# Optimization experiments

Hardware: AMD Instinct MI355X
Metric: run time of the kernel (lower is better)

## Reference

```python
import jax, jax.numpy as jnp
import numpy as np
import math

B, SES, SEQ, H, K = 16, 16, 64, 512, 32
L = SES * SEQ


def setup_inputs() -> dict:
    key = jax.random.key(0)
    ks = jax.random.split(key, 16)
    s = 1.0 / math.sqrt(H)
    return {
        "user_emb": jax.random.normal(ks[0], (B, H), jnp.float32),
        "item_emb": jax.random.normal(ks[1], (B, SES, SEQ, H), jnp.float32),
        "mask": jnp.zeros((B, L, K), jnp.float32),
        "index": jax.random.randint(ks[2], (L, K), 0, L, jnp.int64),
        "Wq": jax.random.normal(ks[3], (H, H), jnp.float32) * s,
        "bq": jnp.zeros((H,), jnp.float32),
        "Wk": jax.random.normal(ks[4], (H, H), jnp.float32) * s,
        "bk": jnp.zeros((H,), jnp.float32),
        "Wv": jax.random.normal(ks[5], (H, H), jnp.float32) * s,
        "bv": jnp.zeros((H,), jnp.float32),
        "Wd": jax.random.normal(ks[6], (H, H), jnp.float32) * s,
        "bd": jnp.zeros((H,), jnp.float32),
        "ln_g": jnp.ones((H,), jnp.float32),
        "ln_b": jnp.zeros((H,), jnp.float32),
    }


def reference(user_emb, item_emb, mask, index, Wq, bq, Wk, bk, Wv, bv, Wd, bd, ln_g, ln_b):
    b, ses, seq, h = item_emb.shape
    l = ses * seq
    item_flat = item_emb.reshape(b, l, h)
    q = user_emb @ Wq.T + bq                       # [B, H]
    k = item_flat @ Wk.T + bk                      # [B, L, H]
    v = item_flat @ Wv.T + bv                      # [B, L, H]
    # scalar query against all L keys, scaled by sqrt(hidden_size)
    scores = jnp.einsum("bh,blh->bl", q, k) / math.sqrt(h)
    scores = scores[:, index] + mask               # gather -> [B, L, K]
    w = jax.nn.softmax(scores, axis=-1)            # [B, L, K]
    vg = v[:, index, :]                            # gather -> [B, L, K, H]
    attn_out = jnp.einsum("blk,blkh->blh", w, vg)  # [B, L, H]
    dense = attn_out @ Wd.T + bd
    x = dense + item_flat                          # residual (dropout = identity, eval)
    mu = jnp.mean(x, axis=-1, keepdims=True)
    var = jnp.var(x, axis=-1, keepdims=True)
    y = (x - mu) / jnp.sqrt(var + 1e-12) * ln_g + ln_b
    return y.reshape(b, ses, seq, h)
```

## Files before the change

### kernel.cpp

```cpp
#include <hip/hip_runtime.h>
#include <math.h>

constexpr int HD   = 512;
constexpr int LL   = 1024;
constexpr int MT   = 16384;
constexpr int KNBR = 32;
constexpr float SCL = 0.04419417382415922f;

typedef __attribute__((ext_vector_type(8))) short  bf16x8;
typedef __attribute__((ext_vector_type(4))) float  f32x4;

__device__ inline float b2f(unsigned short u) {
    union { unsigned int i; float f; } v; v.i = (unsigned int)u << 16; return v.f;
}
__device__ inline float b2f_lo(unsigned int u) {
    union { unsigned int i; float f; } v; v.i = u << 16; return v.f;
}
__device__ inline float b2f_hi(unsigned int u) {
    union { unsigned int i; float f; } v; v.i = u & 0xffff0000u; return v.f;
}
__device__ inline unsigned short f2b(float x) {
    union { float f; unsigned int u; } v; v.f = x;
    unsigned int r = v.u + 0x7fff + ((v.u >> 16) & 1);
    return (unsigned short)(r >> 16);
}

constexpr int PB_CONV_I = 8192;
constexpr int PB_CONV_W = 512;
constexpr int PB_Q      = 2048;

__global__ __launch_bounds__(256) void prep(
    const float* __restrict__ item, const float* __restrict__ Wv,
    const float* __restrict__ Wd, const float* __restrict__ u,
    const float* __restrict__ Wq, const float* __restrict__ bq,
    unsigned short* __restrict__ item_bf, unsigned short* __restrict__ Wv_bf,
    unsigned short* __restrict__ Wd_bf, float* __restrict__ q)
{
    const int blk = blockIdx.x, tid = threadIdx.x;

    if (blk < PB_CONV_I) {
        const int i = blk * 1024 + tid * 4;
        float4 v = *(const float4*)&item[i];
        ushort4 o;
        o.x = f2b(v.x); o.y = f2b(v.y); o.z = f2b(v.z); o.w = f2b(v.w);
        *(ushort4*)&item_bf[i] = o;
        return;
    }
    if (blk < PB_CONV_I + PB_CONV_W) {
        const int n = HD*HD;
        const int i = (blk - PB_CONV_I) * 1024 + tid * 4;
        const float* s; unsigned short* d; int off;
        if (i < n) { s = Wv; d = Wv_bf; off = i; }
        else       { s = Wd; d = Wd_bf; off = i - n; }
        float4 v = *(const float4*)&s[off];
        ushort4 o;
        o.x = f2b(v.x); o.y = f2b(v.y); o.z = f2b(v.z); o.w = f2b(v.w);
        *(ushort4*)&d[off] = o;
        return;
    }
    {
        const int wid  = (blk - PB_CONV_I - PB_CONV_W) * 4 + (tid >> 6);
        const int lane = tid & 63;
        const int b = wid >> 9, h = wid & 511;
        const float* ur = &u[b*HD + lane*8];
        const float* wr = &Wq[(size_t)h*HD + lane*8];
        const float4 u0 = *(const float4*)ur, u1 = *(const float4*)(ur+4);
        const float4 w0 = *(const float4*)wr, w1 = *(const float4*)(wr+4);
        float acc = u0.x*w0.x + u0.y*w0.y + u0.z*w0.z + u0.w*w0.w
                  + u1.x*w1.x + u1.y*w1.y + u1.z*w1.z + u1.w*w1.w;
        #pragma unroll
        for (int off = 32; off; off >>= 1) acc += __shfl_down(acc, off);
        if (lane == 0) q[b*HD + h] = acc + bq[h];
    }
}

__global__ __launch_bounds__(256) void gemm_v_r(
    const unsigned short* __restrict__ A, const unsigned short* __restrict__ W,
    const float* __restrict__ bv, const float* __restrict__ Wk,
    const float* __restrict__ bk, const float* __restrict__ q,
    unsigned short* __restrict__ v_bf, float* __restrict__ rbuf,
    float* __restrict__ s0buf)
{
    __shared__ unsigned short As[2][128 * 32];
    __shared__ unsigned short Bs[2][128 * 32];

    const int blk = blockIdx.x;
    const int tid = threadIdx.x;

    if (blk >= 512) {
        if (blk < 640) {
            __shared__ float red[4][64];
            const int rblk = blk - 512;
            const int b = rblk >> 3, c0 = (rblk & 7) * 64;
            const int cl = tid & 63, hg = tid >> 6;
            const float* qb = &q[b*HD];
            const float* wb = &Wk[(size_t)hg*128*HD + c0 + cl];
            float acc = 0.f;
            #pragma unroll 8
            for (int h = 0; h < 128; h++)
                acc += qb[hg*128 + h] * wb[(size_t)h*HD];
            red[hg][cl] = acc;
            __syncthreads();
            if (tid < 64)
                rbuf[b*HD + c0 + tid] = SCL *
                    (red[0][tid] + red[1][tid] + red[2][tid] + red[3][tid]);
        } else {
            __shared__ float sp[4];
            const int b = blk - 640;
            float p = q[b*HD + tid]*bk[tid] + q[b*HD + tid + 256]*bk[tid + 256];
            #pragma unroll
            for (int off = 32; off; off >>= 1) p += __shfl_down(p, off);
            if ((tid & 63) == 0) sp[tid >> 6] = p;
            __syncthreads();
            if (tid == 0) s0buf[b] = (sp[0] + sp[1] + sp[2] + sp[3]) * SCL;
        }
        return;
    }

    const int rowb = (blk & 7) | ((blk >> 5) << 3);
    const int colb = (blk >> 3) & 3;
    const int row0 = rowb * 128;
    const int col0 = colb * 128;

    const int wave = tid >> 6, lane = tid & 63;
    const int wm = (wave >> 1) * 64;
    const int wn = (wave & 1)  * 64;

    const int lrr = lane >> 2;
    const int cc  = lane & 3;
    int st_row[2], st_gchunk[2];
    #pragma unroll
    for (int t = 0; t < 2; t++) {
        const int m = wave*32 + t*16 + lrr;
        st_row[t]    = m;
        st_gchunk[t] = cc ^ ((m >> 1) & 3);
    }

    const int fr   = lane & 15;
    const int quad = lane >> 4;

    f32x4 acc[4][4];
    #pragma unroll
    for (int i = 0; i < 4; i++)
        #pragma unroll
        for (int j = 0; j < 4; j++)
            acc[i][j] = (f32x4){0.f, 0.f, 0.f, 0.f};

    int a_off[4], b_off[4];
    #pragma unroll
    for (int i = 0; i < 4; i++) {
        const int m = wm + i*16 + fr;
        a_off[i] = m*32 + ((quad ^ ((m >> 1) & 3)) << 3);
        const int n = wn + i*16 + fr;
        b_off[i] = n*32 + ((quad ^ ((n >> 1) & 3)) << 3);
    }

    auto stage = [&](int bf, int k0) {
        #pragma unroll
        for (int t = 0; t < 2; t++) {
            const int m = st_row[t];
            const unsigned short* ga = &A[(size_t)(row0 + m)*HD + k0 + st_gchunk[t]*8];
            __builtin_amdgcn_global_load_lds(
                (const __attribute__((address_space(1))) void*)ga,
                (__attribute__((address_space(3))) void*)&As[bf][(wave*32 + t*16)*32],
                16, 0, 0);
            const unsigned short* gw = &W[(size_t)(col0 + m)*HD + k0 + st_gchunk[t]*8];
            __builtin_amdgcn_global_load_lds(
                (const __attribute__((address_space(1))) void*)gw,
                (__attribute__((address_space(3))) void*)&Bs[bf][(wave*32 + t*16)*32],
                16, 0, 0);
        }
    };

    stage(0, 0);
    __syncthreads();
    int cur = 0;
    for (int k0 = 0; k0 < HD; k0 += 32) {
        if (k0 + 32 < HD) stage(cur ^ 1, k0 + 32);

        bf16x8 af[4], bfr[4];
        #pragma unroll
        for (int i = 0; i < 4; i++) {
            af[i]  = *(const bf16x8*)&As[cur][a_off[i]];
            bfr[i] = *(const bf16x8*)&Bs[cur][b_off[i]];
        }
        #pragma unroll
        for (int i = 0; i < 4; i++)
            #pragma unroll
            for (int j = 0; j < 4; j++)
                acc[i][j] = __builtin_amdgcn_mfma_f32_16x16x32_bf16(
                    af[i], bfr[j], acc[i][j], 0, 0, 0);
        __syncthreads();
        cur ^= 1;
    }

    #pragma unroll
    for (int j = 0; j < 4; j++) {
        const int col = col0 + wn + j*16 + fr;
        const float bb = bv[col];
        #pragma unroll
        for (int i = 0; i < 4; i++) {
            #pragma unroll
            for (int r = 0; r < 4; r++) {
                const int row = row0 + wm + i*16 + quad*4 + r;
                v_bf[(size_t)row*HD + col] = f2b(acc[i][j][r] + bb);
            }
        }
    }
}

__global__ __launch_bounds__(256) void gp_scores(
    const float* __restrict__ rbuf, const float* __restrict__ s0buf,
    const unsigned short* __restrict__ item_bf, float* __restrict__ scores)
{
    const int m = blockIdx.x * 4 + (threadIdx.x >> 6);
    const int lane = threadIdx.x & 63;
    const int b = m >> 10;
    const unsigned short* ir = &item_bf[(size_t)m*HD + lane*8];
    const uint4 iv = *(const uint4*)ir;
    const float* rr = &rbuf[b*HD + lane*8];
    const float4 r0 = *(const float4*)rr;
    const float4 r1 = *(const float4*)(rr + 4);
    float acc = r0.x*b2f_lo(iv.x) + r0.y*b2f_hi(iv.x)
              + r0.z*b2f_lo(iv.y) + r0.w*b2f_hi(iv.y)
              + r1.x*b2f_lo(iv.z) + r1.y*b2f_hi(iv.z)
              + r1.z*b2f_lo(iv.w) + r1.w*b2f_hi(iv.w);
    #pragma unroll
    for (int off = 32; off; off >>= 1) acc += __shfl_down(acc, off);
    if (lane == 0) scores[m] = acc + s0buf[b];
}

__global__ __launch_bounds__(256) void gp_attn(
    const float* __restrict__ scores, const int* __restrict__ index,
    const float* __restrict__ mask, const unsigned short* __restrict__ v,
    unsigned short* __restrict__ attn)
{
    const int bid = blockIdx.x;
    const int m = ((bid & 7) << 11) | ((bid >> 3) << 2) | (int)(threadIdx.x >> 6);
    const int lane = threadIdx.x & 63;
    const int b = m >> 10, l = m & 1023;

    const int t = lane & 31;
    const int idx = index[l*KNBR + t];
    const float s = scores[b*LL + idx] + mask[(size_t)m*KNBR + t];

    float mx = s;
    #pragma unroll
    for (int off = 16; off; off >>= 1) mx = fmaxf(mx, __shfl_xor(mx, off));
    const float e = __expf(s - mx);
    float sum = e;
    #pragma unroll
    for (int off = 16; off; off >>= 1) sum += __shfl_xor(sum, off);
    const float w = e / sum;

    const unsigned short* vbase = v + (size_t)(b << 10) * HD + lane*8;
    float a[8] = {};
    #pragma unroll 8
    for (int t2 = 0; t2 < KNBR; t2++) {
        const int   it = __shfl(idx, t2);
        const float wt = __shfl(w,   t2);
        const uint4 pv = *(const uint4*)(vbase + (size_t)it*HD);
        a[0] += wt * b2f_lo(pv.x); a[1] += wt * b2f_hi(pv.x);
        a[2] += wt * b2f_lo(pv.y); a[3] += wt * b2f_hi(pv.y);
        a[4] += wt * b2f_lo(pv.z); a[5] += wt * b2f_hi(pv.z);
        a[6] += wt * b2f_lo(pv.w); a[7] += wt * b2f_hi(pv.w);
    }
    uint4 o;
    o.x = (unsigned int)f2b(a[0]) | ((unsigned int)f2b(a[1]) << 16);
    o.y = (unsigned int)f2b(a[2]) | ((unsigned int)f2b(a[3]) << 16);
    o.z = (unsigned int)f2b(a[4]) | ((unsigned int)f2b(a[5]) << 16);
    o.w = (unsigned int)f2b(a[6]) | ((unsigned int)f2b(a[7]) << 16);
    *(uint4*)&attn[(size_t)m*HD + lane*8] = o;
}

__global__ __launch_bounds__(256) void dense_ln(
    const unsigned short* __restrict__ A,
    const unsigned short* __restrict__ W,
    const float* __restrict__ bd, const unsigned short* __restrict__ res,
    const float* __restrict__ ln_g, const float* __restrict__ ln_b,
    float* __restrict__ out)
{
    __shared__ unsigned short As[2][32 * 32];
    __shared__ unsigned short Bs[2][512 * 32];
    __shared__ float rsum[4][32], rsq[4][32];

    const int tid  = threadIdx.x;
    const int wave = tid >> 6, lane = tid & 63;
    const int row0 = blockIdx.x * 32;

    const int lrr = lane >> 2;
    const int cc  = lane & 3;
    const int fr   = lane & 15;
    const int quad = lane >> 4;

    f32x4 acc[2][8];
    #pragma unroll
    for (int i = 0; i < 2; i++)
        #pragma unroll
        for (int j = 0; j < 8; j++)
            acc[i][j] = (f32x4){0.f, 0.f, 0.f, 0.f};

    int a_off[2], b_off[8];
    #pragma unroll
    for (int i = 0; i < 2; i++) {
        const int m = i*16 + fr;
        a_off[i] = m*32 + ((quad ^ ((m >> 1) & 3)) << 3);
    }
    #pragma unroll
    for (int j = 0; j < 8; j++) {
        const int n = wave*128 + j*16 + fr;
        b_off[j] = n*32 + ((quad ^ ((n >> 1) & 3)) << 3);
    }

    auto stage = [&](int bf, int k0) {
        #pragma unroll
        for (int t = 0; t < 8; t++) {
            const int n   = wave*128 + t*16 + lrr;
            const int gch = cc ^ ((n >> 1) & 3);
            const unsigned short* gw = &W[(size_t)n*HD + k0 + gch*8];
            __builtin_amdgcn_global_load_lds(
                (const __attribute__((address_space(1))) void*)gw,
                (__attribute__((address_space(3))) void*)&Bs[bf][(wave*128 + t*16)*32],
                16, 0, 0);
        }
        if (wave < 2) {
            const int mm  = wave*16 + lrr;
            const int gch = cc ^ ((mm >> 1) & 3);
            const unsigned short* ga = &A[(size_t)(row0 + mm)*HD + k0 + gch*8];
            __builtin_amdgcn_global_load_lds(
                (const __attribute__((address_space(1))) void*)ga,
                (__attribute__((address_space(3))) void*)&As[bf][(wave*16)*32],
                16, 0, 0);
        }
    };

    stage(0, 0);
    stage(1, 32);

    for (int s = 0; s < 16; ++s) {
        if (wave < 2) asm volatile("s_waitcnt vmcnt(9)" ::: "memory");
        else          asm volatile("s_waitcnt vmcnt(8)" ::: "memory");
        __builtin_amdgcn_s_barrier();
        asm volatile("" ::: "memory");

        const int cur = s & 1;
        bf16x8 af[2], bfr[8];
        #pragma unroll
        for (int i = 0; i < 2; i++) af[i] = *(const bf16x8*)&As[cur][a_off[i]];
        #pragma unroll
        for (int j = 0; j < 8; j++) bfr[j] = *(const bf16x8*)&Bs[cur][b_off[j]];
        asm volatile("s_waitcnt lgkmcnt(0)" ::: "memory");
        __builtin_amdgcn_sched_barrier(0);
        __builtin_amdgcn_s_barrier();

        if (s + 2 < 16) stage(cur, (s + 2) * 32);

        __builtin_amdgcn_s_setprio(1);
        #pragma unroll
        for (int i = 0; i < 2; i++)
            #pragma unroll
            for (int j = 0; j < 8; j++)
                acc[i][j] = __builtin_amdgcn_mfma_f32_16x16x32_bf16(
                    af[i], bfr[j], acc[i][j], 0, 0, 0);
        __builtin_amdgcn_s_setprio(0);
    }
    __syncthreads();

    float bdv[8], gv[8], lbv[8];
    #pragma unroll
    for (int j = 0; j < 8; j++) {
        const int col = wave*128 + j*16 + fr;
        bdv[j] = bd[col]; gv[j] = ln_g[col]; lbv[j] = ln_b[col];
    }

    #pragma unroll
    for (int i = 0; i < 2; i++) {
        #pragma unroll
        for (int r = 0; r < 4; r++) {
            const int lrow = i*16 + quad*4 + r;
            const size_t gr = (size_t)(row0 + lrow) * HD;
            float a1 = 0.f, a2 = 0.f;
            #pragma unroll
            for (int j = 0; j < 8; j++) {
                const int col = wave*128 + j*16 + fr;
                float val = acc[i][j][r] + bdv[j] + b2f(res[gr + col]);
                acc[i][j][r] = val;
                a1 += val; a2 += val*val;
            }
            #pragma unroll
            for (int off = 1; off < 16; off <<= 1) {
                a1 += __shfl_xor(a1, off);
                a2 += __shfl_xor(a2, off);
            }
            if (fr == 0) { rsum[wave][lrow] = a1; rsq[wave][lrow] = a2; }
        }
    }
    __syncthreads();

    #pragma unroll
    for (int i = 0; i < 2; i++) {
        #pragma unroll
        for (int r = 0; r < 4; r++) {
            const int lrow = i*16 + quad*4 + r;
            const float tot  = rsum[0][lrow] + rsum[1][lrow] + rsum[2][lrow] + rsum[3][lrow];
            const float tot2 = rsq[0][lrow]  + rsq[1][lrow]  + rsq[2][lrow]  + rsq[3][lrow];
            const float mu  = tot * (1.f/HD);
            const float var = tot2 * (1.f/HD) - mu*mu;
            const float inv = rsqrtf(var + 1e-12f);
            const size_t gr = (size_t)(row0 + lrow) * HD;
            #pragma unroll
            for (int j = 0; j < 8; j++) {
                const int col = wave*128 + j*16 + fr;
                out[gr + col] = (acc[i][j][r] - mu)*inv*gv[j] + lbv[j];
            }
        }
    }
}

extern "C" void kernel_launch(void* const* d_in, const int* in_sizes, int n_in,
                              void* d_out, int out_size, void* d_ws, size_t ws_size,
                              hipStream_t stream) {
    const float* user_emb = (const float*)d_in[0];
    const float* item_emb = (const float*)d_in[1];
    const float* mask     = (const float*)d_in[2];
    const int*   index    = (const int*)  d_in[3];
    const float* Wq = (const float*)d_in[4];  const float* bq = (const float*)d_in[5];
    const float* Wk = (const float*)d_in[6];  const float* bk = (const float*)d_in[7];
    const float* Wv = (const float*)d_in[8];  const float* bv = (const float*)d_in[9];
    const float* Wd = (const float*)d_in[10]; const float* bd = (const float*)d_in[11];
    const float* ln_g = (const float*)d_in[12];
    const float* ln_b = (const float*)d_in[13];

    float* out = (float*)d_out;

    char* p = (char*)d_ws;
    unsigned short* item_bf = (unsigned short*)p; p += (size_t)MT*HD*2;
    unsigned short* v_bf    = (unsigned short*)p; p += (size_t)MT*HD*2;
    unsigned short* attn_bf = (unsigned short*)p; p += (size_t)MT*HD*2;
    unsigned short* Wv_bf   = (unsigned short*)p; p += (size_t)HD*HD*2;
    unsigned short* Wd_bf   = (unsigned short*)p; p += (size_t)HD*HD*2;
    float* q      = (float*)p; p += 16*HD*4;
    float* rbuf   = (float*)p; p += 16*HD*4;
    float* s0buf  = (float*)p; p += 16*4;
    float* scores = (float*)p; p += MT*4;

    prep<<<PB_CONV_I + PB_CONV_W + PB_Q, 256, 0, stream>>>(
        item_emb, Wv, Wd, user_emb, Wq, bq,
        item_bf, Wv_bf, Wd_bf, q);

    gemm_v_r<<<656, 256, 0, stream>>>(item_bf, Wv_bf, bv, Wk, bk, q,
                                      v_bf, rbuf, s0buf);

    gp_scores<<<MT/4, 256, 0, stream>>>(rbuf, s0buf, item_bf, scores);

    gp_attn<<<MT/4, 256, 0, stream>>>(scores, index, mask, v_bf, attn_bf);

    dense_ln<<<MT/32, 256, 0, stream>>>(attn_bf, Wd_bf, bd, item_bf,
                                        ln_g, ln_b, out);
}
```

Baseline: 184.5 us.

## Pipeline V-projection GEMM with two-deep prefetch, peel last k-steps, use readlane

Rewrites the V-projection GEMM main loop to prefetch two stages ahead. It uses explicit vmcnt waits, split barriers and priority raising around the MFMAs, replacing a single __syncthreads double buffer. The final k-step is peeled out of the loop in both that GEMM and the dense+LN GEMM, so the last iteration can drain with vmcnt(0) instead of relying on the per-wave count waits. The gather kernel broadcasts the neighbour index and weight with readlane instead of shuffles, which saves LDS-permute traffic. The hand-tuned vmcnt counts must match the number of loads in flight, so a wrong count would cause a race.

Result: no change. 183.6 us (-0.5%).

```diff
diff --git a/kernel.cpp b/kernel.cpp
--- a/kernel.cpp
+++ b/kernel.cpp
@@ -173,25 +173,53 @@
     };
 
     stage(0, 0);
-    __syncthreads();
-    int cur = 0;
-    for (int k0 = 0; k0 < HD; k0 += 32) {
-        if (k0 + 32 < HD) stage(cur ^ 1, k0 + 32);
-
+    stage(1, 32);
+
+    for (int s = 0; s < 15; ++s) {
+        asm volatile("s_waitcnt vmcnt(4)" ::: "memory");
+        __builtin_amdgcn_s_barrier();
+        asm volatile("" ::: "memory");
+
+        const int cur = s & 1;
         bf16x8 af[4], bfr[4];
         #pragma unroll
         for (int i = 0; i < 4; i++) {
             af[i]  = *(const bf16x8*)&As[cur][a_off[i]];
             bfr[i] = *(const bf16x8*)&Bs[cur][b_off[i]];
         }
+        asm volatile("s_waitcnt lgkmcnt(0)" ::: "memory");
+        __builtin_amdgcn_sched_barrier(0);
+        __builtin_amdgcn_s_barrier();
+
+        if (s + 2 < 16) stage(cur, (s + 2) * 32);
+
+        __builtin_amdgcn_s_setprio(1);
         #pragma unroll
         for (int i = 0; i < 4; i++)
             #pragma unroll
             for (int j = 0; j < 4; j++)
                 acc[i][j] = __builtin_amdgcn_mfma_f32_16x16x32_bf16(
                     af[i], bfr[j], acc[i][j], 0, 0, 0);
-        __syncthreads();
-        cur ^= 1;
+        __builtin_amdgcn_s_setprio(0);
+    }
+    {
+        asm volatile("s_waitcnt vmcnt(0)" ::: "memory");
+        __builtin_amdgcn_s_barrier();
+        asm volatile("" ::: "memory");
+        bf16x8 af[4], bfr[4];
+        #pragma unroll
+        for (int i = 0; i < 4; i++) {
+            af[i]  = *(const bf16x8*)&As[1][a_off[i]];
+            bfr[i] = *(const bf16x8*)&Bs[1][b_off[i]];
+        }
+        asm volatile("s_waitcnt lgkmcnt(0)" ::: "memory");
+        __builtin_amdgcn_sched_barrier(0);
+        #pragma unroll
+        for (int i = 0; i < 4; i++)
+            #pragma unroll
+            for (int j = 0; j < 4; j++)
+                acc[i][j] = __builtin_amdgcn_mfma_f32_16x16x32_bf16(
+                    af[i], bfr[j], acc[i][j], 0, 0, 0);
     }
 
     #pragma unroll
@@ -253,13 +281,15 @@
     for (int off = 16; off; off >>= 1) sum += __shfl_xor(sum, off);
     const float w = e / sum;
 
-    const unsigned short* vbase = v + (size_t)(b << 10) * HD + lane*8;
+    const unsigned short* vb = v + (size_t)(b << 10) * HD;
+    const int loff = lane * 8;
     float a[8] = {};
     #pragma unroll 8
     for (int t2 = 0; t2 < KNBR; t2++) {
-        const int   it = __shfl(idx, t2);
-        const float wt = __shfl(w,   t2);
-        const uint4 pv = *(const uint4*)(vbase + (size_t)it*HD);
+        const int   it = __builtin_amdgcn_readlane(idx, t2);
+        const float wt = __int_as_float(
+            __builtin_amdgcn_readlane(__float_as_int(w), t2));
+        const uint4 pv = *(const uint4*)(vb + (size_t)it*HD + loff);
         a[0] += wt * b2f_lo(pv.x); a[1] += wt * b2f_hi(pv.x);
         a[2] += wt * b2f_lo(pv.y); a[3] += wt * b2f_hi(pv.y);
         a[4] += wt * b2f_lo(pv.z); a[5] += wt * b2f_hi(pv.z);
@@ -337,7 +367,7 @@
     stage(0, 0);
     stage(1, 32);
 
-    for (int s = 0; s < 16; ++s) {
+    for (int s = 0; s < 15; ++s) {
         if (wave < 2) asm volatile("s_waitcnt vmcnt(9)" ::: "memory");
         else          asm volatile("s_waitcnt vmcnt(8)" ::: "memory");
         __builtin_amdgcn_s_barrier();
@@ -363,6 +393,24 @@
                 acc[i][j] = __builtin_amdgcn_mfma_f32_16x16x32_bf16(
                     af[i], bfr[j], acc[i][j], 0, 0, 0);
         __builtin_amdgcn_s_setprio(0);
+    }
+    {
+        asm volatile("s_waitcnt vmcnt(0)" ::: "memory");
+        __builtin_amdgcn_s_barrier();
+        asm volatile("" ::: "memory");
+        bf16x8 af[2], bfr[8];
+        #pragma unroll
+        for (int i = 0; i < 2; i++) af[i] = *(const bf16x8*)&As[1][a_off[i]];
+        #pragma unroll
+        for (int j = 0; j < 8; j++) bfr[j] = *(const bf16x8*)&Bs[1][b_off[j]];
+        asm volatile("s_waitcnt lgkmcnt(0)" ::: "memory");
+        __builtin_amdgcn_sched_barrier(0);
+        #pragma unroll
+        for (int i = 0; i < 2; i++)
+            #pragma unroll
+            for (int j = 0; j < 8; j++)
+                acc[i][j] = __builtin_amdgcn_mfma_f32_16x16x32_bf16(
+                    af[i], bfr[j], acc[i][j], 0, 0, 0);
     }
     __syncthreads();
 
```
